# Optimization experiments

Measured on AMD Instinct MI355X. Metric: run time of the kernel, lower is better.

The kernel has to match this reference:

```python
import jax, jax.numpy as jnp
import numpy as np

EMBED_DIM = 1024
LAMBDA_INIT = 0.8
EPS = 1e-5


def setup_inputs() -> dict:
    key = jax.random.key(0)
    ks = jax.random.split(key, 8)
    D = EMBED_DIM
    x = jax.random.normal(ks[0], (4, 2048, D), dtype=jnp.float32)
    # torch Linear weight [out, in]; we store transposed [in, out] for x @ W
    s = 1.0 / np.sqrt(D)
    w_q12 = jax.random.uniform(ks[1], (D, 2 * D), jnp.float32, -s, s)
    w_k12 = jax.random.uniform(ks[2], (D, 2 * D), jnp.float32, -s, s)
    w_v = jax.random.uniform(ks[3], (D, D), jnp.float32, -s, s)
    lambda_q1 = 0.1 * jax.random.normal(ks[4], (D,), jnp.float32)
    lambda_k1 = 0.1 * jax.random.normal(ks[5], (D,), jnp.float32)
    lambda_q2 = 0.1 * jax.random.normal(ks[6], (D,), jnp.float32)
    lambda_k2 = 0.1 * jax.random.normal(ks[7], (D,), jnp.float32)
    return {"x": x, "w_q12": w_q12, "w_k12": w_k12, "w_v": w_v,
            "lambda_q1": lambda_q1, "lambda_k1": lambda_k1,
            "lambda_q2": lambda_q2, "lambda_k2": lambda_k2}


def reference(x, w_q12, w_k12, w_v, lambda_q1, lambda_k1, lambda_q2, lambda_k2):
    D = x.shape[-1]
    scale = D ** (-0.25)
    q12 = jnp.einsum('bsd,de->bse', x, w_q12)
    k12 = jnp.einsum('bsd,de->bse', x, w_k12)
    q1, q2 = jnp.split(q12, 2, axis=-1)
    k1, k2 = jnp.split(k12, 2, axis=-1)
    v = jnp.einsum('bsd,de->bse', x, w_v)
    attn1 = jnp.einsum('bqd,bkd->bqk', q1, k1) * scale
    attn2 = jnp.einsum('bqd,bkd->bqk', q2, k2) * scale
    lam1 = jnp.exp(jnp.sum(lambda_q1 * lambda_k1))
    lam2 = jnp.exp(jnp.sum(lambda_q2 * lambda_k2))
    lam_full = lam1 - lam2 + LAMBDA_INIT
    diff = jax.nn.softmax(attn1, axis=-1) - lam_full * jax.nn.softmax(attn2, axis=-1)
    out = jnp.einsum('bqk,bkd->bqd', diff, v)
    # RMSNorm (no affine), then scale by (1 - lambda_init)
    rms = jnp.sqrt(jnp.mean(out * out, axis=-1, keepdims=True) + EPS)
    return (out / rms) * (1.0 - LAMBDA_INIT)
```

## Files before the change

kernel.cpp:

```cpp
#include <hip/hip_runtime.h>

typedef float f32x4 __attribute__((ext_vector_type(4)));
typedef _Float16 h16x8 __attribute__((ext_vector_type(8)));
typedef _Float16 h16x4 __attribute__((ext_vector_type(4)));

#define GLOAD_LDS16(gp, lp) __builtin_amdgcn_global_load_lds(               \
    (const __attribute__((address_space(1))) void*)(gp),                    \
    (__attribute__((address_space(3))) void*)(lp), 16, 0, 0)

#define BARX do { __builtin_amdgcn_s_barrier(); asm volatile("" ::: "memory"); } while (0)
#define VMW(N) asm volatile("s_waitcnt vmcnt(" #N ")" ::: "memory")

__global__ __launch_bounds__(256) void cast_x(const float* __restrict__ x,
                                              _Float16* __restrict__ xh) {
  long i = (long)blockIdx.x * 256 + threadIdx.x;
  f32x4 a = *(const f32x4*)(x + i * 8);
  f32x4 b = *(const f32x4*)(x + i * 8 + 4);
  h16x8 h;
  h[0] = (_Float16)a[0]; h[1] = (_Float16)a[1];
  h[2] = (_Float16)a[2]; h[3] = (_Float16)a[3];
  h[4] = (_Float16)b[0]; h[5] = (_Float16)b[1];
  h[6] = (_Float16)b[2]; h[7] = (_Float16)b[3];
  *(h16x8*)(xh + i * 8) = h;
}

__global__ __launch_bounds__(256) void tcw(const float* __restrict__ in,
                                           _Float16* __restrict__ out,
                                           int Kd, int Nd, float scale) {
  __shared__ float tile[64][65];
  const int t = threadIdx.x;
  const int k0 = blockIdx.y * 64, n0 = blockIdx.x * 64;
  const int tr = t >> 4, tc = (t & 15) * 4;
#pragma unroll
  for (int i = 0; i < 4; ++i) {
    int r = i * 16 + tr;
    f32x4 a = *(const f32x4*)(in + (long)(k0 + r) * Nd + n0 + tc);
    tile[r][tc + 0] = a[0]; tile[r][tc + 1] = a[1];
    tile[r][tc + 2] = a[2]; tile[r][tc + 3] = a[3];
  }
  __syncthreads();
#pragma unroll
  for (int i = 0; i < 4; ++i) {
    int r = i * 16 + tr;
    h16x4 h;
#pragma unroll
    for (int q = 0; q < 4; ++q) h[q] = (_Float16)(tile[tc + q][r] * scale);
    *(h16x4*)(out + (long)(n0 + r) * Kd + k0 + tc) = h;
  }
}

__global__ __launch_bounds__(256) void trans16(const _Float16* __restrict__ in,
                                               _Float16* __restrict__ out,
                                               int R, int Cd, long ibatch, long obatch) {
  __shared__ _Float16 tile[64][72];
  in += (long)blockIdx.z * ibatch;
  out += (long)blockIdx.z * obatch;
  const int t = threadIdx.x;
  const int r0 = blockIdx.y * 64, c0 = blockIdx.x * 64;
  const int tr = t >> 3, tc8 = (t & 7) * 8;
#pragma unroll
  for (int i = 0; i < 2; ++i) {
    int r = i * 32 + tr;
    h16x8 a = *(const h16x8*)(in + (long)(r0 + r) * Cd + c0 + tc8);
    *(h16x8*)(&tile[r][tc8]) = a;
  }
  __syncthreads();
#pragma unroll
  for (int i = 0; i < 2; ++i) {
    int r = i * 32 + tr;
    h16x8 h;
#pragma unroll
    for (int q = 0; q < 8; ++q) h[q] = tile[tc8 + q][r];
    *(h16x8*)(out + (long)(c0 + r) * R + r0 + tc8) = h;
  }
}

__global__ __launch_bounds__(1024) void lambda_k(const float* __restrict__ lq1,
                                                 const float* __restrict__ lk1,
                                                 const float* __restrict__ lq2,
                                                 const float* __restrict__ lk2,
                                                 float* __restrict__ lam) {
  __shared__ float sh1[16], sh2[16];
  const int t = threadIdx.x;
  float p1 = lq1[t] * lk1[t];
  float p2 = lq2[t] * lk2[t];
#pragma unroll
  for (int off = 1; off < 64; off <<= 1) {
    p1 += __shfl_xor(p1, off);
    p2 += __shfl_xor(p2, off);
  }
  if ((t & 63) == 0) { sh1[t >> 6] = p1; sh2[t >> 6] = p2; }
  __syncthreads();
  if (t == 0) {
    float s1 = 0.f, s2 = 0.f;
    for (int i = 0; i < 16; ++i) { s1 += sh1[i]; s2 += sh2[i]; }
    lam[0] = __expf(s1) - __expf(s2) + 0.8f;
  }
}

template <int NREP, typename CT>
__global__ __launch_bounds__(512, 2) void g8(
    const _Float16* __restrict__ A, const _Float16* __restrict__ B,
    CT* __restrict__ C, int K, int lda, int ldb, int ldc,
    long abatch, long bbatch, long cbatch, long a2, long c2, int natt,
    int nbx, int nby) {
  constexpr int BN = NREP * 64;
  constexpr int BNH = BN / 2;
  constexpr int NH = NREP / 2;
  __shared__ _Float16 As[2][2][128 * 64];
  __shared__ _Float16 Bs[2][2][BNH * 64];

  const int nwg = gridDim.x;
  const int orig = blockIdx.x;
  const int qd = nwg >> 3, rm = nwg & 7;
  const int xcd = orig & 7, sub_ = orig >> 3;
  const int wgid = (xcd < rm ? xcd * (qd + 1) : rm * (qd + 1) + (xcd - rm) * qd) + sub_;

  const int z = wgid / (nbx * nby);
  const int rem = wgid - z * nbx * nby;
  const int by = rem / nbx;
  const int bx = rem - by * nbx;
  const int att = z % natt;
  const int bz = z / natt;

  const int t = threadIdx.x;
  const int lane = t & 63, wv = t >> 6;
  const int wm = wv >> 2, wn = wv & 3;
  const int lg = lane >> 4, l15 = lane & 15;

  const _Float16* Ab = A + (long)bz * abatch + (long)att * a2 + (long)(by * 256) * lda;
  const _Float16* Bb = B + (long)bz * bbatch + (long)att * a2 + (long)(bx * BN) * ldb;

  auto stgA = [&](int T, int s) {
    const int db = T & 1;
#pragma unroll
    for (int j = 0; j < 2; ++j) {
      const int c = t + j * 512;
      const int ru = c >> 3, p = c & 7;
      const int gs = p ^ (ru & 7);
      const int grow = (ru < 64) ? (s * 64 + ru) : (128 + s * 64 + (ru - 64));
      GLOAD_LDS16(Ab + (long)grow * lda + T * 64 + gs * 8, &As[db][s][c * 8]);
    }
  };
  auto stgB = [&](int T, int s) {
    const int db = T & 1;
#pragma unroll
    for (int j = 0; j < (NREP == 4 ? 2 : 1); ++j) {
      const int c = t + j * 512;
      const int ru = c >> 3, p = c & 7;
      const int gs = p ^ (ru & 7);
      GLOAD_LDS16(Bb + (long)(s * BNH + ru) * ldb + T * 64 + gs * 8, &Bs[db][s][c * 8]);
    }
  };

  int swz[2];
  swz[0] = ((lg) ^ (l15 & 7)) * 16;
  swz[1] = ((4 + lg) ^ (l15 & 7)) * 16;

  h16x8 fA[4][2], fB0[NH][2], fB1[NH][2];
  f32x4 acc[8][NREP] = {};

  auto rdA = [&](int db, int s) {
    const char* base = (const char*)&As[db][s][0] + (wm * 64 + l15) * 128;
#pragma unroll
    for (int j = 0; j < 4; ++j) {
      fA[j][0] = *(const h16x8*)(base + j * 2048 + swz[0]);
      fA[j][1] = *(const h16x8*)(base + j * 2048 + swz[1]);
    }
  };
  auto rdB = [&](int db, int s, h16x8 (&dst)[NH][2]) {
    const char* base = (const char*)&Bs[db][s][0] + (wn * (BNH / 4) + l15) * 128;
#pragma unroll
    for (int j = 0; j < NH; ++j) {
      dst[j][0] = *(const h16x8*)(base + j * 2048 + swz[0]);
      dst[j][1] = *(const h16x8*)(base + j * 2048 + swz[1]);
    }
  };
  auto QUAD = [&](int ms, int ns, h16x8 (&fb)[NH][2]) {
    __builtin_amdgcn_s_setprio(1);
#pragma unroll
    for (int j = 0; j < 4; ++j)
#pragma unroll
      for (int n = 0; n < NH; ++n) {
        acc[ms * 4 + j][ns * NH + n] = __builtin_amdgcn_mfma_f32_16x16x32_f16(
            fA[j][0], fb[n][0], acc[ms * 4 + j][ns * NH + n], 0, 0, 0);
        acc[ms * 4 + j][ns * NH + n] = __builtin_amdgcn_mfma_f32_16x16x32_f16(
            fA[j][1], fb[n][1], acc[ms * 4 + j][ns * NH + n], 0, 0, 0);
      }
    __builtin_amdgcn_s_setprio(0);
  };

  const int NT = K >> 6;

  stgB(0, 0); stgA(0, 0); stgB(0, 1); stgA(0, 1); stgB(1, 0); stgA(1, 0); stgB(1, 1);
  if constexpr (NREP == 4) VMW(6); else VMW(4);
  BARX;

  for (int T = 0; T + 2 < NT; T += 2) {
    rdA(0, 0); rdB(0, 0, fB0); stgA(T + 1, 1);
    BARX; QUAD(0, 0, fB0); BARX;
    rdB(0, 1, fB1); stgB(T + 2, 0);
    BARX; QUAD(0, 1, fB1); BARX;
    rdA(0, 1); stgA(T + 2, 0);
    BARX; QUAD(1, 1, fB1); BARX;
    stgB(T + 2, 1);
    if constexpr (NREP == 4) VMW(6); else VMW(4);
    BARX; QUAD(1, 0, fB0); BARX;
    rdA(1, 0); rdB(1, 0, fB0); stgA(T + 2, 1);
    BARX; QUAD(0, 0, fB0); BARX;
    rdB(1, 1, fB1); stgB(T + 3, 0);
    BARX; QUAD(0, 1, fB1); BARX;
    rdA(1, 1); stgA(T + 3, 0);
    BARX; QUAD(1, 1, fB1); BARX;
    stgB(T + 3, 1);
    if constexpr (NREP == 4) VMW(6); else VMW(4);
    BARX; QUAD(1, 0, fB0); BARX;
  }

  {
    rdA(0, 0); rdB(0, 0, fB0); stgA(NT - 1, 1);
    BARX; QUAD(0, 0, fB0); BARX;
    rdB(0, 1, fB1);
    BARX; QUAD(0, 1, fB1); BARX;
    rdA(0, 1);
    BARX; QUAD(1, 1, fB1); BARX;
    VMW(0);
    BARX; QUAD(1, 0, fB0); BARX;
    rdA(1, 0); rdB(1, 0, fB0);
    BARX; QUAD(0, 0, fB0); BARX;
    rdB(1, 1, fB1);
    BARX; QUAD(0, 1, fB1); BARX;
    rdA(1, 1);
    BARX; QUAD(1, 1, fB1); BARX;
    QUAD(1, 0, fB0);
  }

  CT* Cb = C + (long)bz * cbatch + (long)att * c2;
  const int crow0 = by * 256 + wm * 128;
  const int ccol0 = bx * BN + wn * (BNH / 4);
#pragma unroll
  for (int ms = 0; ms < 2; ++ms)
#pragma unroll
    for (int j = 0; j < 4; ++j)
#pragma unroll
      for (int ns = 0; ns < 2; ++ns)
#pragma unroll
        for (int n = 0; n < NH; ++n)
#pragma unroll
          for (int q = 0; q < 4; ++q) {
            const int row = crow0 + ms * 64 + j * 16 + lg * 4 + q;
            const int col = ccol0 + ns * BNH + n * 16 + l15;
            Cb[(long)row * ldc + col] = (CT)acc[ms * 4 + j][ns * NH + n][q];
          }
}

__global__ __launch_bounds__(256) void softmax_diff(const _Float16* __restrict__ S1,
                                                    const _Float16* __restrict__ S2,
                                                    _Float16* __restrict__ D,
                                                    const float* __restrict__ lamp) {
  const long row = (long)blockIdx.x * 4 + (threadIdx.x >> 6);
  const int lane = threadIdx.x & 63;
  const float lam = *lamp;
  const _Float16* s1 = S1 + row * 2048;
  const _Float16* s2 = S2 + row * 2048;
  float v1[32], v2[32];
  float m1 = -3e38f, m2 = -3e38f;
#pragma unroll
  for (int j = 0; j < 4; ++j) {
    h16x8 a = ((const h16x8*)s1)[j * 64 + lane];
    h16x8 b = ((const h16x8*)s2)[j * 64 + lane];
#pragma unroll
    for (int q = 0; q < 8; ++q) {
      v1[j * 8 + q] = (float)a[q]; v2[j * 8 + q] = (float)b[q];
      m1 = fmaxf(m1, v1[j * 8 + q]); m2 = fmaxf(m2, v2[j * 8 + q]);
    }
  }
#pragma unroll
  for (int off = 1; off < 64; off <<= 1) {
    m1 = fmaxf(m1, __shfl_xor(m1, off));
    m2 = fmaxf(m2, __shfl_xor(m2, off));
  }
  float l1 = 0.f, l2 = 0.f;
#pragma unroll
  for (int e = 0; e < 32; ++e) {
    v1[e] = __expf(v1[e] - m1); l1 += v1[e];
    v2[e] = __expf(v2[e] - m2); l2 += v2[e];
  }
#pragma unroll
  for (int off = 1; off < 64; off <<= 1) {
    l1 += __shfl_xor(l1, off);
    l2 += __shfl_xor(l2, off);
  }
  const float r1 = 1.f / l1, r2 = lam / l2;
  _Float16* d = D + row * 2048;
#pragma unroll
  for (int j = 0; j < 4; ++j) {
    h16x8 h;
#pragma unroll
    for (int q = 0; q < 8; ++q)
      h[q] = (_Float16)(v1[j * 8 + q] * r1 - v2[j * 8 + q] * r2);
    ((h16x8*)d)[j * 64 + lane] = h;
  }
}

__global__ __launch_bounds__(256) void rmsnorm(const _Float16* __restrict__ O,
                                               float* __restrict__ out) {
  const long row = (long)blockIdx.x * 4 + (threadIdx.x >> 6);
  const int lane = threadIdx.x & 63;
  const _Float16* o = O + row * 1024;
  h16x8 a = ((const h16x8*)o)[lane];
  h16x8 b = ((const h16x8*)o)[64 + lane];
  float xa[8], xb[8];
  float ss = 0.f;
#pragma unroll
  for (int q = 0; q < 8; ++q) {
    xa[q] = (float)a[q]; xb[q] = (float)b[q];
    ss += xa[q] * xa[q] + xb[q] * xb[q];
  }
#pragma unroll
  for (int off = 1; off < 64; off <<= 1) ss += __shfl_xor(ss, off);
  const float s = 0.2f * rsqrtf(ss * (1.f / 1024.f) + 1e-5f);
  float* po = out + row * 1024;
  f32x4 r;
#pragma unroll
  for (int q = 0; q < 4; ++q) r[q] = xa[q] * s;
  *(f32x4*)(po + lane * 8) = r;
#pragma unroll
  for (int q = 0; q < 4; ++q) r[q] = xa[4 + q] * s;
  *(f32x4*)(po + lane * 8 + 4) = r;
#pragma unroll
  for (int q = 0; q < 4; ++q) r[q] = xb[q] * s;
  *(f32x4*)(po + 512 + lane * 8) = r;
#pragma unroll
  for (int q = 0; q < 4; ++q) r[q] = xb[4 + q] * s;
  *(f32x4*)(po + 512 + lane * 8 + 4) = r;
}

extern "C" void kernel_launch(void* const* d_in, const int* in_sizes, int n_in,
                              void* d_out, int out_size, void* d_ws, size_t ws_size,
                              hipStream_t stream) {
  const float* x   = (const float*)d_in[0];
  const float* wq  = (const float*)d_in[1];
  const float* wk  = (const float*)d_in[2];
  const float* wv  = (const float*)d_in[3];
  const float* lq1 = (const float*)d_in[4];
  const float* lk1 = (const float*)d_in[5];
  const float* lq2 = (const float*)d_in[6];
  const float* lk2 = (const float*)d_in[7];
  float* out = (float*)d_out;

  const size_t MB = 1ull << 20;
  char* ws = (char*)d_ws;
  _Float16* xh   = (_Float16*)(ws + 0);
  _Float16* Wp   = (_Float16*)(ws + 16 * MB);
  _Float16* qkv  = (_Float16*)(ws + 26 * MB);
  _Float16* vt   = (_Float16*)(ws + 106 * MB);
  _Float16* S1   = (_Float16*)(ws + 122 * MB);
  _Float16* S2   = (_Float16*)(ws + 154 * MB);
  float*    lam  = (float*)(ws + 186 * MB);
  _Float16* diff = (_Float16*)(ws + 26 * MB);
  _Float16* opre = (_Float16*)(ws + 58 * MB);

  const float scale = 0.17677669529663689f;

  cast_x<<<4096, 256, 0, stream>>>(x, xh);
  tcw<<<dim3(32, 16), 256, 0, stream>>>(wq, Wp, 1024, 2048, scale);
  tcw<<<dim3(32, 16), 256, 0, stream>>>(wk, Wp + 2048l * 1024, 1024, 2048, 1.0f);
  tcw<<<dim3(16, 16), 256, 0, stream>>>(wv, Wp + 4096l * 1024, 1024, 1024, 1.0f);
  lambda_k<<<1, 1024, 0, stream>>>(lq1, lk1, lq2, lk2, lam);

  g8<4, _Float16><<<640, 512, 0, stream>>>(xh, Wp, qkv, 1024, 1024, 1024, 5120,
                                           0, 0, 0, 0, 0, 1, 20, 32);

  trans16<<<dim3(16, 32, 4), 256, 0, stream>>>(qkv + 4096, vt, 2048, 5120,
                                               2048l * 5120, 1024l * 2048);

  g8<4, _Float16><<<512, 512, 0, stream>>>(qkv, qkv + 2048, S1, 1024, 5120, 5120, 2048,
                                           2048l * 5120, 2048l * 5120, 2048l * 2048,
                                           1024, 16777216l, 2, 8, 8);

  softmax_diff<<<2048, 256, 0, stream>>>(S1, S2, diff, lam);

  g8<2, _Float16><<<256, 512, 0, stream>>>(diff, vt, opre, 2048, 2048, 2048, 1024,
                                           2048l * 2048, 1024l * 2048, 2048l * 1024,
                                           0, 0, 1, 8, 8);

  rmsnorm<<<2048, 256, 0, stream>>>(opre, out);
}
```

Measured before the change: 271.7 us.

## Add 256-thread 256x256-tile triple-buffered GEMM for QKV and score matmuls

Adds a new GEMM kernel with 256x256 output tiles computed by 4 waves, each holding an 8x8 grid of 16x16 MFMA accumulators. It uses a K step of 32 with a three-slot LDS ring loaded via global_load_lds and a swizzled layout, and it is used for the QKV projection and the two attention-score GEMMs. The goal is more data reuse per LDS load and deeper prefetch than the previous 512-thread g8 kernel. In exchange each thread holds 256 accumulator registers at one workgroup per CU, so occupancy is low, and the epilogue writes C with scalar 16-bit stores.

```diff
diff --git a/kernel.cpp b/kernel.cpp
--- a/kernel.cpp
+++ b/kernel.cpp
@@ -96,6 +96,103 @@
     for (int i = 0; i < 16; ++i) { s1 += sh1[i]; s2 += sh2[i]; }
     lam[0] = __expf(s1) - __expf(s2) + 0.8f;
   }
+}
+
+template <typename CT>
+__global__ __launch_bounds__(256, 1) void gemmt(
+    const _Float16* __restrict__ A, const _Float16* __restrict__ B,
+    CT* __restrict__ C, int K, int lda, int ldb, int ldc,
+    long abatch, long bbatch, long cbatch, long a2, long c2, int natt,
+    int nbx, int nby) {
+  __shared__ _Float16 As[3][256 * 32];
+  __shared__ _Float16 Bs[3][256 * 32];
+
+  const int nwg = gridDim.x;
+  const int orig = blockIdx.x;
+  const int qd = nwg >> 3, rm = nwg & 7;
+  const int xcd = orig & 7, sub = orig >> 3;
+  const int wgid = (xcd < rm ? xcd * (qd + 1) : rm * (qd + 1) + (xcd - rm) * qd) + sub;
+
+  const int z = wgid / (nbx * nby);
+  const int rem = wgid - z * nbx * nby;
+  const int by = rem / nbx;
+  const int bx = rem - by * nbx;
+  const int att = z % natt;
+  const int bz = z / natt;
+
+  const int t = threadIdx.x;
+  const int lane = t & 63, wv = t >> 6;
+  const int wm = wv >> 1, wn = wv & 1;
+  const int lg = lane >> 4, l15 = lane & 15;
+
+  const _Float16* Ab = A + (long)bz * abatch + (long)att * a2 + (long)(by * 256) * lda;
+  const _Float16* Bb = B + (long)bz * bbatch + (long)att * a2 + (long)(bx * 256) * ldb;
+
+  auto stage = [&](int slot, int S) {
+    const long ko = (long)S * 32;
+#pragma unroll
+    for (int j = 0; j < 4; ++j) {
+      const int e = t + j * 256;
+      const int r = e >> 2;
+      const int gs = ((e & 3) - (r >> 1)) & 3;
+      GLOAD_LDS16(Ab + (long)r * lda + ko + gs * 8, &As[slot][e * 8]);
+      GLOAD_LDS16(Bb + (long)r * ldb + ko + gs * 8, &Bs[slot][e * 8]);
+    }
+  };
+
+  int offA[8], offB[8];
+#pragma unroll
+  for (int m = 0; m < 8; ++m) {
+    const int r = wm * 128 + m * 16 + l15;
+    offA[m] = (r * 4 + ((lg + (r >> 1)) & 3)) * 8;
+  }
+#pragma unroll
+  for (int n = 0; n < 8; ++n) {
+    const int r = wn * 128 + n * 16 + l15;
+    offB[n] = (r * 4 + ((lg + (r >> 1)) & 3)) * 8;
+  }
+
+  f32x4 acc[8][8] = {};
+  const int NS = K >> 5;
+
+  stage(0, 0); stage(1, 1);
+  int cur = 0, nx2 = 2;
+
+  for (int S = 0; S < NS; ++S) {
+    if (S == NS - 1) VMW(0);
+    else VMW(8);
+    BARX;
+
+    if (S + 2 < NS) stage(nx2, S + 2);
+
+    const _Float16* Ap = &As[cur][0];
+    const _Float16* Bp = &Bs[cur][0];
+    h16x8 a[8], b[8];
+#pragma unroll
+    for (int m = 0; m < 8; ++m) a[m] = *(const h16x8*)(Ap + offA[m]);
+#pragma unroll
+    for (int n = 0; n < 8; ++n) b[n] = *(const h16x8*)(Bp + offB[n]);
+#pragma unroll
+    for (int m = 0; m < 8; ++m)
+#pragma unroll
+      for (int n = 0; n < 8; ++n)
+        acc[m][n] = __builtin_amdgcn_mfma_f32_16x16x32_f16(a[m], b[n], acc[m][n], 0, 0, 0);
+
+    cur = (cur == 2) ? 0 : cur + 1;
+    nx2 = (nx2 == 2) ? 0 : nx2 + 1;
+  }
+
+  CT* Cb = C + (long)bz * cbatch + (long)att * c2;
+  const int crow0 = by * 256 + wm * 128;
+  const int ccol0 = bx * 256 + wn * 128;
+#pragma unroll
+  for (int m = 0; m < 8; ++m)
+#pragma unroll
+    for (int n = 0; n < 8; ++n)
+#pragma unroll
+      for (int j = 0; j < 4; ++j)
+        Cb[(long)(crow0 + m * 16 + lg * 4 + j) * ldc + ccol0 + n * 16 + l15] =
+            (CT)acc[m][n][j];
 }
 
 template <int NREP, typename CT>
@@ -369,13 +466,13 @@
   tcw<<<dim3(16, 16), 256, 0, stream>>>(wv, Wp + 4096l * 1024, 1024, 1024, 1.0f);
   lambda_k<<<1, 1024, 0, stream>>>(lq1, lk1, lq2, lk2, lam);
 
-  g8<4, _Float16><<<640, 512, 0, stream>>>(xh, Wp, qkv, 1024, 1024, 1024, 5120,
+  gemmt<_Float16><<<640, 256, 0, stream>>>(xh, Wp, qkv, 1024, 1024, 1024, 5120,
                                            0, 0, 0, 0, 0, 1, 20, 32);
 
   trans16<<<dim3(16, 32, 4), 256, 0, stream>>>(qkv + 4096, vt, 2048, 5120,
                                                2048l * 5120, 1024l * 2048);
 
-  g8<4, _Float16><<<512, 512, 0, stream>>>(qkv, qkv + 2048, S1, 1024, 5120, 5120, 2048,
+  gemmt<_Float16><<<512, 256, 0, stream>>>(qkv, qkv + 2048, S1, 1024, 5120, 5120, 2048,
                                            2048l * 5120, 2048l * 5120, 2048l * 2048,
                                            1024, 16777216l, 2, 8, 8);
 
```

Result: slower. 350.6 us (+29.0%).
